# Kernel optimization log

Measured on AMD Instinct MI355X. Metric: run time of the kernel, lower is better.

The kernel has to match this reference:

```python
import jax, jax.numpy as jnp
import numpy as np
from jax import lax

B, C, H, W = 4, 256, 96, 96
DR, G, KS, RF = 4, 2, 3, 9.0
HID = C // DR          # 64
GC = HID // G          # 32 (group_channel)
SCALE = HID ** -0.5
MLP_H = C * 4          # 1024
EPS = 1e-5


def conv2d(x, w, b=None, groups=1):
    out = lax.conv_general_dilated(x, w, (1, 1), 'SAME',
                                   dimension_numbers=('NCHW', 'OIHW', 'NCHW'),
                                   feature_group_count=groups)
    return out if b is None else out + b[None, :, None, None]


def ln_chw(x, g, b):  # LayerNormProxy: layernorm over channel dim of NCHW
    m = x.mean(1, keepdims=True)
    v = ((x - m) ** 2).mean(1, keepdims=True)
    return (x - m) / jnp.sqrt(v + EPS) * g[None, :, None, None] + b[None, :, None, None]


def ln_last(x, g, b):
    m = x.mean(-1, keepdims=True)
    v = ((x - m) ** 2).mean(-1, keepdims=True)
    return (x - m) / jnp.sqrt(v + EPS) * g + b


def base_offset():
    pad = (KS - 1) // 2
    base = jnp.arange(-pad, pad + 1, dtype=jnp.float32)
    by = jnp.repeat(base, KS)
    bx = jnp.tile(base, KS)
    return jnp.stack([by, bx], 1).reshape(1, -1, 1, 1)  # [1, 2*KS*KS, 1, 1], (kh kw d) layout


def bilinear_zeros(img, ry, rx):
    # img [Cc,H,W]; ry,rx absolute pixel coords [Ho,Wo]; zero padding, align_corners=True
    Hh, Ww = img.shape[1], img.shape[2]
    y0 = jnp.floor(ry); x0 = jnp.floor(rx)
    wy = ry - y0; wx = rx - x0
    y0i = y0.astype(jnp.int32); x0i = x0.astype(jnp.int32)

    def corner(yi, xi, w):
        valid = (yi >= 0) & (yi < Hh) & (xi >= 0) & (xi < Ww)
        yc = jnp.clip(yi, 0, Hh - 1); xc = jnp.clip(xi, 0, Ww - 1)
        return img[:, yc, xc] * (w * valid)[None]

    return (corner(y0i, x0i, (1 - wy) * (1 - wx)) + corner(y0i, x0i + 1, (1 - wy) * wx)
            + corner(y0i + 1, x0i, wy * (1 - wx)) + corner(y0i + 1, x0i + 1, wy * wx))


def extract_feats(img, off):
    # img [(b g), Cc, H, W], off [(b g), 2*KS*KS, H, W] -> [(b g), KS*KS, Cc, H, W]
    Bg, Cc = img.shape[0], img.shape[1]
    off = off.reshape(Bg, KS, KS, 2, H, W).transpose(0, 1, 4, 2, 5, 3)  # b kh h kw w d
    iy, ix = jnp.meshgrid(jnp.arange(H, dtype=off.dtype), jnp.arange(W, dtype=off.dtype), indexing='ij')
    idx = jnp.stack([iy, ix], -1)  # [H, W, 2]
    coords = (off + idx[None, None, :, None]).reshape(Bg, KS * H, KS * W, 2)
    # torch normalizes to [-1,1] then grid_sample(align_corners=True) un-normalizes => absolute coords
    samp = jax.vmap(bilinear_zeros)(img, coords[..., 0], coords[..., 1])  # [Bg, Cc, KS*H, KS*W]
    return samp.reshape(Bg, Cc, KS, H, KS, W).transpose(0, 2, 4, 1, 3, 5).reshape(Bg, KS * KS, Cc, H, W)


def ldca_forward(x, y, g11, b11, g21, b21, g12, b12, w_qkv1, w_qkv2,
                 off1_dw_w, off1_ln_g, off1_ln_b, off1_w, off1_b,
                 off2_dw_w, off2_ln_g, off2_ln_b, off2_w, off2_b,
                 rpb, proj_w, proj_b, fc1_w, fc1_b, dw_w, dw_b, fc2_w, fc2_b):
    x_ = ln_chw(x, g11, b11)
    y_ = ln_chw(y, g21, b21)
    qkv1 = jnp.einsum('oc,bchw->bohw', w_qkv1, x_)   # [B, 3*HID, H, W]
    kv2c = jnp.einsum('oc,bchw->bohw', w_qkv2, y_)   # [B, 2*HID, H, W]
    q1 = qkv1[:, :HID].reshape(B * G, GC, H, W)

    def regroup(kv):  # b (d g c) h w -> (b g) (d c) h w
        return kv.reshape(B, 2, G, GC, H, W).transpose(0, 2, 1, 3, 4, 5).reshape(B * G, 2 * GC, H, W)

    kv1 = regroup(qkv1[:, HID:])
    kv2 = regroup(kv2c)

    bo = base_offset()

    def off_branch(dww, lng, lnb, w, b):
        t = conv2d(q1, dww, None, groups=GC)
        t = jax.nn.gelu(ln_chw(t, lng, lnb), approximate=False)
        return jnp.tanh(conv2d(t, w, b)) * RF + bo

    s1 = extract_feats(kv1, off_branch(off1_dw_w, off1_ln_g, off1_ln_b, off1_w, off1_b))
    s2 = extract_feats(kv2, off_branch(off2_dw_w, off2_ln_g, off2_ln_b, off2_w, off2_b))

    def to_kv(s):  # (b g) n (d c) h w -> d b (h w) n (g c)
        return s.reshape(B, G, KS * KS, 2, GC, H, W).transpose(3, 0, 5, 6, 2, 1, 4).reshape(2, B, H * W, KS * KS, G * GC)

    k1, v1 = to_kv(s1)
    k2, v2 = to_kv(s2)
    k = jnp.concatenate([k1 + rpb, k2 + rpb], 2)   # [B, HW, 2*KS*KS, HID]
    v = jnp.concatenate([v1, v2], 2)
    q = q1.reshape(B, G, GC, H, W).transpose(0, 3, 4, 1, 2).reshape(B, H * W, 1, G * GC) * SCALE
    attn = jax.nn.softmax(jnp.einsum('bnqd,bnkd->bnqk', q, k), axis=-1)
    o = jnp.einsum('bnqk,bnkd->bnqd', attn, v)[:, :, 0]  # [B, HW, HID]
    o = o @ proj_w.T + proj_b + x.transpose(0, 2, 3, 1).reshape(B, H * W, C)
    # MLP with depthwise-conv branch
    h = ln_last(o, g12, b12) @ fc1_w.T + fc1_b           # [B, HW, MLP_H]
    hd = conv2d(h.transpose(0, 2, 1).reshape(B, MLP_H, H, W), dw_w, dw_b, groups=MLP_H)
    hd = hd.reshape(B, MLP_H, H * W).transpose(0, 2, 1)
    h = jax.nn.gelu(h + hd, approximate=False)
    o = o + h @ fc2_w.T + fc2_b
    return o.reshape(B, H, W, C).transpose(0, 3, 1, 2)


def setup_inputs() -> dict:
    key = jax.random.key(0)
    keys = iter(jax.random.split(key, 40))

    def nrm(shape, s=0.02):
        return jax.random.normal(next(keys), shape, jnp.float32) * s

    inp = {
        'x': jax.random.normal(next(keys), (B, C, H, W), jnp.float32),
        'y': jax.random.normal(next(keys), (B, C, H, W), jnp.float32),
        'g11': jnp.ones((C,), jnp.float32), 'b11': jnp.zeros((C,), jnp.float32),
        'g21': jnp.ones((C,), jnp.float32), 'b21': jnp.zeros((C,), jnp.float32),
        'g12': jnp.ones((C,), jnp.float32), 'b12': jnp.zeros((C,), jnp.float32),
        'w_qkv1': nrm((3 * HID, C)), 'w_qkv2': nrm((2 * HID, C)),
        'off1_dw_w': nrm((GC, 1, 3, 3)),
        'off1_ln_g': jnp.ones((GC,), jnp.float32), 'off1_ln_b': jnp.zeros((GC,), jnp.float32),
        'off1_w': nrm((2 * KS * KS, GC, 3, 3)), 'off1_b': jnp.zeros((2 * KS * KS,), jnp.float32),
        'off2_dw_w': nrm((GC, 1, 3, 3)),
        'off2_ln_g': jnp.ones((GC,), jnp.float32), 'off2_ln_b': jnp.zeros((GC,), jnp.float32),
        'off2_w': nrm((2 * KS * KS, GC, 3, 3)), 'off2_b': jnp.zeros((2 * KS * KS,), jnp.float32),
        'rpb': nrm((1, 1, KS * KS, HID)),
        'proj_w': nrm((C, HID)), 'proj_b': jnp.zeros((C,), jnp.float32),
        'fc1_w': nrm((MLP_H, C)), 'fc1_b': jnp.zeros((MLP_H,), jnp.float32),
        'dw_w': nrm((MLP_H, 1, 3, 3)), 'dw_b': jnp.zeros((MLP_H,), jnp.float32),
        'fc2_w': nrm((C, MLP_H)), 'fc2_b': jnp.zeros((C,), jnp.float32),
    }
    return inp


def reference(x, y, g11, b11, g21, b21, g12, b12, w_qkv1, w_qkv2,
              off1_dw_w, off1_ln_g, off1_ln_b, off1_w, off1_b,
              off2_dw_w, off2_ln_g, off2_ln_b, off2_w, off2_b,
              rpb, proj_w, proj_b, fc1_w, fc1_b, dw_w, dw_b, fc2_w, fc2_b):
    return ldca_forward(x, y, g11, b11, g21, b21, g12, b12, w_qkv1, w_qkv2,
                        off1_dw_w, off1_ln_g, off1_ln_b, off1_w, off1_b,
                        off2_dw_w, off2_ln_g, off2_ln_b, off2_w, off2_b,
                        rpb, proj_w, proj_b, fc1_w, fc1_b, dw_w, dw_b, fc2_w, fc2_b)
```

## Files before the change

kernel.cpp:

```cpp
#include <hip/hip_runtime.h>
#include <math.h>


#define HH 96
#define WWD 96
#define HWP 9216
#define EPSV 1e-5f
#define RFV 9.0f

typedef unsigned short ushort;
typedef __attribute__((ext_vector_type(8))) short short8v;
typedef __attribute__((ext_vector_type(8))) ushort ushort8v;
typedef __attribute__((ext_vector_type(4))) float f32x4;

__device__ inline ushort f2bf(float f) {
  union { float f; unsigned u; } v; v.f = f;
  unsigned r = v.u + 0x7FFFu + ((v.u >> 16) & 1u);
  return (ushort)(r >> 16);
}
__device__ inline float bf2f(ushort h) {
  union { unsigned u; float f; } v; v.u = ((unsigned)h) << 16;
  return v.f;
}

__device__ inline void stf(float* p, float v) { *p = v; }
__device__ inline void stf(ushort* p, float v) { *p = f2bf(v); }

__device__ inline void stage16(const float* __restrict__ s, ushort* d) {
  const float4* s4 = (const float4*)s;
  float4 v0 = s4[0], v1 = s4[1], v2 = s4[2], v3 = s4[3];
  ushort8v r0, r1;
  r0[0] = f2bf(v0.x); r0[1] = f2bf(v0.y); r0[2] = f2bf(v0.z); r0[3] = f2bf(v0.w);
  r0[4] = f2bf(v1.x); r0[5] = f2bf(v1.y); r0[6] = f2bf(v1.z); r0[7] = f2bf(v1.w);
  r1[0] = f2bf(v2.x); r1[1] = f2bf(v2.y); r1[2] = f2bf(v2.z); r1[3] = f2bf(v2.w);
  r1[4] = f2bf(v3.x); r1[5] = f2bf(v3.y); r1[6] = f2bf(v3.z); r1[7] = f2bf(v3.w);
  ((ushort8v*)d)[0] = r0; ((ushort8v*)d)[1] = r1;
}
__device__ inline void stage16(const ushort* __restrict__ s, ushort* d) {
  ((ushort8v*)d)[0] = ((const ushort8v*)s)[0];
  ((ushort8v*)d)[1] = ((const ushort8v*)s)[1];
}

__global__ __launch_bounds__(256) void k_ln_stats(const float* __restrict__ in,
                                                  float* __restrict__ mout,
                                                  float* __restrict__ rout, int Cn) {
  int idx = blockIdx.x * 256 + threadIdx.x;
  int b = idx / HWP, p = idx % HWP;
  const float* base = in + (size_t)b * Cn * HWP + p;
  float s = 0.f, ss = 0.f;
  for (int c = 0; c < Cn; ++c) { float v = base[(size_t)c * HWP]; s += v; ss += v * v; }
  float m = s / (float)Cn;
  float var = ss / (float)Cn - m * m;
  mout[idx] = m;
  rout[idx] = rsqrtf(var + EPSV);
}

__global__ __launch_bounds__(256) void k_ln_stats_cc(const float* __restrict__ in,
                                                     float* __restrict__ mout,
                                                     float* __restrict__ rout) {
  int px = blockIdx.x * 4 + (threadIdx.x >> 6);
  int lane = threadIdx.x & 63;
  float4 v = *(const float4*)(in + (size_t)px * 256 + lane * 4);
  float s = v.x + v.y + v.z + v.w;
  float ss = v.x * v.x + v.y * v.y + v.z * v.z + v.w * v.w;
#pragma unroll
  for (int d = 1; d < 64; d <<= 1) { s += __shfl_xor(s, d); ss += __shfl_xor(ss, d); }
  if (lane == 0) {
    float m = s / 256.f;
    mout[px] = m;
    rout[px] = rsqrtf(ss / 256.f - m * m + EPSV);
  }
}

__global__ __launch_bounds__(256) void k_prepbf(const float* __restrict__ w,
                                                const float* __restrict__ g,
                                                const float* __restrict__ beta,
                                                ushort* __restrict__ wbf,
                                                float* __restrict__ sg, float* __restrict__ wb,
                                                int O, int K, int scaleRows) {
  int o = blockIdx.x * 4 + (threadIdx.x >> 6);
  int lane = threadIdx.x & 63;
  if (o >= O) return;
  float sc = (o < scaleRows) ? 0.125f : 1.f;
  float sgv = 0.f, wbv = 0.f;
  for (int c = lane; c < K; c += 64) {
    float wv = w[(size_t)o * K + c];
    float t = wv * (g ? g[c] : 1.f) * sc;
    ushort u = f2bf(t);
    wbf[(size_t)o * K + c] = u;
    sgv += bf2f(u);
    wbv += wv * (beta ? beta[c] : 0.f);
  }
#pragma unroll
  for (int d = 1; d < 64; d <<= 1) { sgv += __shfl_xor(sgv, d); wbv += __shfl_xor(wbv, d); }
  if (lane == 0) {
    if (sg) sg[o] = sgv;
    if (wb) wb[o] = wbv * sc;
  }
}

__global__ __launch_bounds__(256) void k_tocc(const float* __restrict__ src,
                                              ushort* __restrict__ dst) {
  __shared__ float tile[64][65];
  int tp = threadIdx.x & 63, tq = threadIdx.x >> 6;
  int p0 = blockIdx.x * 64, c0 = blockIdx.y * 64, b = blockIdx.z;
#pragma unroll 4
  for (int i = 0; i < 16; ++i) {
    int ch = tq * 16 + i;
    tile[ch][tp] = src[((size_t)b * 256 + c0 + ch) * HWP + p0 + tp];
  }
  __syncthreads();
#pragma unroll 4
  for (int i = 0; i < 16; ++i) {
    int pp = tq * 16 + i;
    dst[((size_t)b * HWP + p0 + pp) * 256 + c0 + tp] = f2bf(tile[tp][pp]);
  }
}

template <typename TI, typename TO, bool LNF, bool RES>
__global__ __launch_bounds__(256) void k_gemmB(const TI* __restrict__ act,
                                               const ushort* __restrict__ Wbf,
                                               const float* __restrict__ ms,
                                               const float* __restrict__ rs,
                                               const float* __restrict__ sg,
                                               const float* __restrict__ wb,
                                               const float* __restrict__ bias,
                                               const ushort* __restrict__ resid,
                                               TO* __restrict__ outp, int K, int O) {
  __shared__ ushort at[128][56];
  __shared__ ushort wt[64][56];
  int tid = threadIdx.x;
  int lane = tid & 63, wv = tid >> 6;
  int wr = wv >> 1, wc = wv & 1;
  int p0 = blockIdx.x * 128, o0 = blockIdx.y * 64, b = blockIdx.z;
  size_t pb = (size_t)b * HWP;
  int l15 = lane & 15, lk = (lane >> 4) * 8;
  f32x4 acc[4][2];
#pragma unroll
  for (int rt = 0; rt < 4; ++rt)
#pragma unroll
    for (int ct = 0; ct < 2; ++ct) { acc[rt][ct][0] = 0.f; acc[rt][ct][1] = 0.f; acc[rt][ct][2] = 0.f; acc[rt][ct][3] = 0.f; }

  for (int kb = 0; kb < K; kb += 32) {
    __syncthreads();
    {
      int p = tid >> 1, kh = (tid & 1) * 16;
      stage16(act + (pb + p0 + p) * (size_t)K + kb + kh, &at[p][kh]);
    }
    if (tid < 128) {
      int o = tid >> 1, kh = (tid & 1) * 16;
      stage16(Wbf + (size_t)(o0 + o) * K + kb + kh, &wt[o][kh]);
    }
    __syncthreads();
    short8v a[4], bb[2];
#pragma unroll
    for (int rt = 0; rt < 4; ++rt) a[rt] = *(const short8v*)&at[wr * 64 + rt * 16 + l15][lk];
#pragma unroll
    for (int ct = 0; ct < 2; ++ct) bb[ct] = *(const short8v*)&wt[wc * 32 + ct * 16 + l15][lk];
#pragma unroll
    for (int rt = 0; rt < 4; ++rt)
#pragma unroll
      for (int ct = 0; ct < 2; ++ct)
        acc[rt][ct] = __builtin_amdgcn_mfma_f32_16x16x32_bf16(a[rt], bb[ct], acc[rt][ct], 0, 0, 0);
  }
#pragma unroll
  for (int rt = 0; rt < 4; ++rt) {
    int pbase = p0 + wr * 64 + rt * 16 + (lane >> 4) * 4;
#pragma unroll
    for (int j = 0; j < 4; ++j) {
      int p = pbase + j;
      float rr = 0.f, mm = 0.f;
      if (LNF) { rr = rs[b * HWP + p]; mm = ms[b * HWP + p]; }
#pragma unroll
      for (int ct = 0; ct < 2; ++ct) {
        int o = o0 + wc * 32 + ct * 16 + l15;
        float v = acc[rt][ct][j];
        if (LNF) v = rr * v - rr * mm * sg[o];
        if (wb) v += wb[o];
        if (bias) v += bias[o];
        if (RES) v += bf2f(resid[(pb + p) * (size_t)O + o]);
        stf(&outp[(pb + p) * (size_t)O + o], v);
      }
    }
  }
}

__global__ __launch_bounds__(256) void k_q1p(const float* __restrict__ qkv1cc,
                                             float* __restrict__ q1p) {
  __shared__ float tile[64][65];
  int tp = threadIdx.x & 63, tq = threadIdx.x >> 6;
  int p0 = blockIdx.x * 64, b = blockIdx.y;
#pragma unroll 4
  for (int i = 0; i < 16; ++i) {
    int pp = tq * 16 + i;
    tile[tp][pp] = qkv1cc[((size_t)b * HWP + p0 + pp) * 192 + tp];
  }
  __syncthreads();
#pragma unroll 4
  for (int i = 0; i < 16; ++i) {
    int ch = tq * 16 + i;
    q1p[((size_t)b * 64 + ch) * HWP + p0 + tp] = tile[ch][tp] * 8.f;
  }
}

__global__ __launch_bounds__(256) void k_dw3x3(const float* __restrict__ q1p,
                                               const float* __restrict__ dww1,
                                               const float* __restrict__ dww2,
                                               float* __restrict__ t) {
  int p = blockIdx.x * 256 + threadIdx.x;
  int c = blockIdx.y, z = blockIdx.z;
  int bg = z & 7;
  int b = bg >> 1, g = bg & 1;
  const float* dww = (z >= 8) ? dww2 : dww1;
  int y = p / WWD, x = p % WWD;
  const float* src = q1p + ((size_t)b * 64 + g * 32 + c) * HWP;
  float acc = 0.f;
#pragma unroll
  for (int ky = 0; ky < 3; ++ky) {
    int yy = y + ky - 1;
    if (yy < 0 || yy >= HH) continue;
#pragma unroll
    for (int kx = 0; kx < 3; ++kx) {
      int xx = x + kx - 1;
      if (xx < 0 || xx >= WWD) continue;
      acc += src[yy * WWD + xx] * dww[c * 9 + ky * 3 + kx];
    }
  }
  t[(size_t)(z * 32 + c) * HWP + p] = acc;
}

__global__ __launch_bounds__(256) void k_ln_gelu32(float* __restrict__ t,
                                                   const float* __restrict__ g1,
                                                   const float* __restrict__ b1,
                                                   const float* __restrict__ g2,
                                                   const float* __restrict__ b2) {
  int idx = blockIdx.x * 256 + threadIdx.x;
  int z = idx / HWP, p = idx % HWP;
  const float* g = (z >= 8) ? g2 : g1;
  const float* bb = (z >= 8) ? b2 : b1;
  float* base = t + (size_t)z * 32 * HWP + p;
  float s = 0.f, ss = 0.f;
#pragma unroll
  for (int c = 0; c < 32; ++c) { float v = base[(size_t)c * HWP]; s += v; ss += v * v; }
  float m = s / 32.f;
  float var = ss / 32.f - m * m;
  float r = rsqrtf(var + EPSV);
#pragma unroll
  for (int c = 0; c < 32; ++c) {
    float v = base[(size_t)c * HWP];
    float xn = (v - m) * r * g[c] + bb[c];
    base[(size_t)c * HWP] = 0.5f * xn * (1.f + erff(xn * 0.70710678118654752f));
  }
}

__global__ __launch_bounds__(256) void k_conv18(const float* __restrict__ t,
                                                const float* __restrict__ w1,
                                                const float* __restrict__ b1,
                                                const float* __restrict__ w2,
                                                const float* __restrict__ b2,
                                                float* __restrict__ offo) {
  __shared__ float in_t[32 * 324];
  int tid = threadIdx.x;
  int tile = blockIdx.x, z = blockIdx.y;
  int ty0 = (tile / 6) * 16, tx0 = (tile % 6) * 16;
  const float* w = (z >= 8) ? w2 : w1;
  const float* bias = (z >= 8) ? b2 : b1;
  const float* tb = t + (size_t)z * 32 * HWP;
  for (int idx = tid; idx < 32 * 324; idx += 256) {
    int c = idx / 324, pp = idx % 324;
    int gy = ty0 - 1 + pp / 18, gx = tx0 - 1 + pp % 18;
    float v = 0.f;
    if (gy >= 0 && gy < HH && gx >= 0 && gx < WWD) v = tb[(size_t)c * HWP + gy * WWD + gx];
    in_t[idx] = v;
  }
  __syncthreads();
  int ly = tid >> 4, lx = tid & 15;
  float acc[18];
#pragma unroll
  for (int oc = 0; oc < 18; ++oc) acc[oc] = bias[oc];
  const float* basep = in_t + ly * 18 + lx;
  for (int c = 0; c < 32; ++c) {
#pragma unroll
    for (int dy = 0; dy < 3; ++dy)
#pragma unroll
      for (int dx = 0; dx < 3; ++dx) {
        float v = basep[c * 324 + dy * 18 + dx];
        int tap = c * 9 + dy * 3 + dx;
#pragma unroll
        for (int oc = 0; oc < 18; ++oc)
          acc[oc] = fmaf(v, w[oc * 288 + tap], acc[oc]);
      }
  }
  int p = (ty0 + ly) * WWD + tx0 + lx;
#pragma unroll
  for (int oc = 0; oc < 18; ++oc) {
    int n = oc >> 1, d = oc & 1;
    float basev = d ? (float)(n % 3 - 1) : (float)(n / 3 - 1);
    offo[((size_t)z * 18 + oc) * HWP + p] = tanhf(acc[oc]) * RFV + basev;
  }
}

__global__ __launch_bounds__(256) void k_attn(const float* __restrict__ qkv1cc,
                                              const float* __restrict__ kv2cc,
                                              const float* __restrict__ offo,
                                              const float* __restrict__ rpb,
                                              float* __restrict__ o_att) {
  __shared__ float rl[576];
  for (int i = threadIdx.x; i < 576; i += 256) rl[i] = rpb[i];
  __syncthreads();
  int pix = blockIdx.x * 4 + (threadIdx.x >> 6);
  int l = threadIdx.x & 63;
  int b = pix / HWP, p = pix % HWP;
  int y = p / WWD, x = p % WWD;
  int g = l >> 5;
  int bg = b * 2 + g;
  float qv = qkv1cc[((size_t)b * HWP + p) * 192 + l];
  float scores[18], vvv[18];
#pragma unroll
  for (int s = 0; s < 2; ++s) {
    const float* offp = offo + ((size_t)(s * 8 + bg) * 18) * HWP + p;
    const float* kvb = s ? (kv2cc + (size_t)b * HWP * 128) : (qkv1cc + (size_t)b * HWP * 192);
    int stride = s ? 128 : 192;
    int koff = s ? 0 : 64;
#pragma unroll
    for (int n = 0; n < 9; ++n) {
      float ry = (float)y + offp[(size_t)(2 * n) * HWP];
      float rx = (float)x + offp[(size_t)(2 * n + 1) * HWP];
      float y0f = floorf(ry), x0f = floorf(rx);
      float wy = ry - y0f, wx = rx - x0f;
      int y0 = (int)y0f, x0 = (int)x0f;
      float ka = 0.f, va = 0.f;
#pragma unroll
      for (int cy = 0; cy < 2; ++cy) {
        int yi = y0 + cy;
        if (yi < 0 || yi >= HH) continue;
        float wyc = cy ? wy : 1.f - wy;
#pragma unroll
        for (int cx = 0; cx < 2; ++cx) {
          int xi = x0 + cx;
          if (xi < 0 || xi >= WWD) continue;
          float wgt = wyc * (cx ? wx : 1.f - wx);
          const float* row = kvb + (size_t)(yi * WWD + xi) * stride + koff;
          ka += wgt * row[l];
          va += wgt * row[64 + l];
        }
      }
      float sp = qv * (ka + rl[n * 64 + l]);
      sp += __shfl_xor(sp, 1);
      sp += __shfl_xor(sp, 2);
      sp += __shfl_xor(sp, 4);
      sp += __shfl_xor(sp, 8);
      sp += __shfl_xor(sp, 16);
      sp += __shfl_xor(sp, 32);
      scores[s * 9 + n] = sp;
      vvv[s * 9 + n] = va;
    }
  }
  float mx = scores[0];
#pragma unroll
  for (int i = 1; i < 18; ++i) mx = fmaxf(mx, scores[i]);
  float sum = 0.f;
#pragma unroll
  for (int i = 0; i < 18; ++i) { scores[i] = expf(scores[i] - mx); sum += scores[i]; }
  float inv = 1.f / sum;
  float o = 0.f;
#pragma unroll
  for (int i = 0; i < 18; ++i) o += scores[i] * vvv[i];
  o_att[((size_t)b * HWP + p) * 64 + l] = o * inv;
}

__global__ __launch_bounds__(256) void k_dwgelu_cc(const ushort* __restrict__ h,
                                                   const float* __restrict__ w,
                                                   const float* __restrict__ bias,
                                                   ushort* __restrict__ h2) {
  __shared__ ushort tileh[324][48];
  __shared__ float wl[32][9];
  __shared__ float bl[32];
  int tid = threadIdx.x;
  int tile = blockIdx.x, chb = blockIdx.y, b = blockIdx.z;
  int ty0 = (tile / 6) * 16, tx0 = (tile % 6) * 16;
  size_t base = ((size_t)b * HWP) * 1024 + chb * 32;
  for (int i = tid; i < 288; i += 256) wl[i / 9][i % 9] = w[(chb * 32 + i / 9) * 9 + i % 9];
  if (tid < 32) bl[tid] = bias[chb * 32 + tid];
  for (int idx = tid; idx < 324; idx += 256) {
    int py = idx / 18, px = idx % 18;
    int gy = ty0 - 1 + py, gx = tx0 - 1 + px;
    ushort8v* d = (ushort8v*)&tileh[idx][0];
    if (gy >= 0 && gy < HH && gx >= 0 && gx < WWD) {
      const ushort8v* sv = (const ushort8v*)(h + base + (size_t)(gy * WWD + gx) * 1024);
      d[0] = sv[0]; d[1] = sv[1]; d[2] = sv[2]; d[3] = sv[3];
    } else {
      ushort8v z;
#pragma unroll
      for (int e = 0; e < 8; ++e) z[e] = 0;
      d[0] = z; d[1] = z; d[2] = z; d[3] = z;
    }
  }
  __syncthreads();
  int ly = tid >> 4, lx = tid & 15;
  float a[32];
#pragma unroll
  for (int c = 0; c < 32; ++c) a[c] = bl[c];
#pragma unroll
  for (int dy = 0; dy < 3; ++dy)
#pragma unroll
    for (int dx = 0; dx < 3; ++dx) {
      const ushort8v* t = (const ushort8v*)&tileh[(ly + dy) * 18 + lx + dx][0];
      int tap = dy * 3 + dx;
#pragma unroll
      for (int cq = 0; cq < 4; ++cq) {
        ushort8v vv = t[cq];
#pragma unroll
        for (int e = 0; e < 8; ++e) a[cq * 8 + e] += bf2f(vv[e]) * wl[cq * 8 + e][tap];
      }
    }
  const ushort8v* ctr = (const ushort8v*)&tileh[(ly + 1) * 18 + lx + 1][0];
  ushort8v* outv = (ushort8v*)(h2 + base + (size_t)((ty0 + ly) * WWD + tx0 + lx) * 1024);
#pragma unroll
  for (int cq = 0; cq < 4; ++cq) {
    ushort8v vv = ctr[cq];
    ushort8v rv;
#pragma unroll
    for (int e = 0; e < 8; ++e) {
      float v = bf2f(vv[e]) + a[cq * 8 + e];
      rv[e] = f2bf(0.5f * v * (1.f + erff(v * 0.70710678118654752f)));
    }
    outv[cq] = rv;
  }
}

__global__ __launch_bounds__(256) void k_fromcc(const float* __restrict__ fc2cc,
                                                const float* __restrict__ o1cc,
                                                float* __restrict__ outp) {
  __shared__ float tile[64][65];
  int tp = threadIdx.x & 63, tq = threadIdx.x >> 6;
  int p0 = blockIdx.x * 64, c0 = blockIdx.y * 64, b = blockIdx.z;
#pragma unroll 4
  for (int i = 0; i < 16; ++i) {
    int pp = tq * 16 + i;
    size_t idx = ((size_t)b * HWP + p0 + pp) * 256 + c0 + tp;
    tile[tp][pp] = fc2cc[idx] + o1cc[idx];
  }
  __syncthreads();
#pragma unroll 4
  for (int i = 0; i < 16; ++i) {
    int ch = tq * 16 + i;
    outp[((size_t)b * 256 + c0 + ch) * HWP + p0 + tp] = tile[ch][tp];
  }
}

extern "C" void kernel_launch(void* const* d_in, const int* in_sizes, int n_in,
                              void* d_out, int out_size, void* d_ws, size_t ws_size,
                              hipStream_t stream) {
  const float* x      = (const float*)d_in[0];
  const float* y      = (const float*)d_in[1];
  const float* g11    = (const float*)d_in[2];
  const float* b11    = (const float*)d_in[3];
  const float* g21    = (const float*)d_in[4];
  const float* b21    = (const float*)d_in[5];
  const float* g12    = (const float*)d_in[6];
  const float* b12    = (const float*)d_in[7];
  const float* w_qkv1 = (const float*)d_in[8];
  const float* w_qkv2 = (const float*)d_in[9];
  const float* o1dw   = (const float*)d_in[10];
  const float* o1lg   = (const float*)d_in[11];
  const float* o1lb   = (const float*)d_in[12];
  const float* o1w    = (const float*)d_in[13];
  const float* o1bi   = (const float*)d_in[14];
  const float* o2dw   = (const float*)d_in[15];
  const float* o2lg   = (const float*)d_in[16];
  const float* o2lb   = (const float*)d_in[17];
  const float* o2w    = (const float*)d_in[18];
  const float* o2bi   = (const float*)d_in[19];
  const float* rpb    = (const float*)d_in[20];
  const float* proj_w = (const float*)d_in[21];
  const float* proj_b = (const float*)d_in[22];
  const float* fc1_w  = (const float*)d_in[23];
  const float* fc1_b  = (const float*)d_in[24];
  const float* dw_w   = (const float*)d_in[25];
  const float* dw_b   = (const float*)d_in[26];
  const float* fc2_w  = (const float*)d_in[27];
  const float* fc2_b  = (const float*)d_in[28];
  float* out = (float*)d_out;

  float* ws = (float*)d_ws;
  ushort* xcc   = (ushort*)(ws + 0);
  ushort* ycc   = (ushort*)(ws + 4718592);
  float*  q1p   = ws + 4718592;
  float*  qkv1cc= ws + 9437184;
  float*  kv2cc = ws + 16515072;
  float*  offb  = ws + 21233664;
  float*  o_att = ws + 23887872;
  float*  tbuf12= ws + 26247168;
  ushort* hcc   = (ushort*)(ws + 0);
  ushort* h2cc  = (ushort*)(ws + 18874368);
  float*  o1cc  = ws + 37748736;
  float*  fc2cc = ws + 0;
  const size_t SW = 47185920;
  float* m_x = ws + SW, *r_x = m_x + 36864, *m_y = r_x + 36864, *r_y = m_y + 36864;
  float* m_o = r_y + 36864, *r_o = m_o + 36864;
  ushort* Wg1bf = (ushort*)(ws + SW + 221184);
  float* sg1 = ws + SW + 245760, *wb1 = sg1 + 192;
  ushort* Wg2bf = (ushort*)(ws + SW + 246144);
  float* sg2 = ws + SW + 262528, *wb2 = sg2 + 128;
  ushort* Wgfbf = (ushort*)(ws + SW + 262784);
  float* sgf = ws + SW + 393856, *wbf = sgf + 1024;
  ushort* projbf = (ushort*)(ws + SW + 395904);
  ushort* fc2bf  = (ushort*)(ws + SW + 404096);

  k_prepbf<<<48, 256, 0, stream>>>(w_qkv1, g11, b11, Wg1bf, sg1, wb1, 192, 256, 64);
  k_prepbf<<<32, 256, 0, stream>>>(w_qkv2, g21, b21, Wg2bf, sg2, wb2, 128, 256, 0);
  k_prepbf<<<256, 256, 0, stream>>>(fc1_w, g12, b12, Wgfbf, sgf, wbf, 1024, 256, 0);
  k_prepbf<<<64, 256, 0, stream>>>(proj_w, nullptr, nullptr, projbf, nullptr, nullptr, 256, 64, 0);
  k_prepbf<<<64, 256, 0, stream>>>(fc2_w, nullptr, nullptr, fc2bf, nullptr, nullptr, 256, 1024, 0);

  k_ln_stats<<<144, 256, 0, stream>>>(x, m_x, r_x, 256);
  k_ln_stats<<<144, 256, 0, stream>>>(y, m_y, r_y, 256);
  k_tocc<<<dim3(144, 4, 4), 256, 0, stream>>>(x, xcc);
  k_tocc<<<dim3(144, 4, 4), 256, 0, stream>>>(y, ycc);

  k_gemmB<ushort, float, true, false><<<dim3(72, 3, 4), 256, 0, stream>>>(
      xcc, Wg1bf, m_x, r_x, sg1, wb1, nullptr, nullptr, qkv1cc, 256, 192);
  k_gemmB<ushort, float, true, false><<<dim3(72, 2, 4), 256, 0, stream>>>(
      ycc, Wg2bf, m_y, r_y, sg2, wb2, nullptr, nullptr, kv2cc, 256, 128);

  k_q1p<<<dim3(144, 4), 256, 0, stream>>>(qkv1cc, q1p);
  k_dw3x3<<<dim3(36, 32, 16), 256, 0, stream>>>(q1p, o1dw, o2dw, tbuf12);
  k_ln_gelu32<<<576, 256, 0, stream>>>(tbuf12, o1lg, o1lb, o2lg, o2lb);
  k_conv18<<<dim3(36, 16), 256, 0, stream>>>(tbuf12, o1w, o1bi, o2w, o2bi, offb);

  k_attn<<<9216, 256, 0, stream>>>(qkv1cc, kv2cc, offb, rpb, o_att);

  k_gemmB<float, float, false, true><<<dim3(72, 4, 4), 256, 0, stream>>>(
      o_att, projbf, nullptr, nullptr, nullptr, nullptr, proj_b, xcc, o1cc, 64, 256);

  k_ln_stats_cc<<<9216, 256, 0, stream>>>(o1cc, m_o, r_o);
  k_gemmB<float, ushort, true, false><<<dim3(72, 16, 4), 256, 0, stream>>>(
      o1cc, Wgfbf, m_o, r_o, sgf, wbf, fc1_b, nullptr, hcc, 256, 1024);
  k_dwgelu_cc<<<dim3(36, 32, 4), 256, 0, stream>>>(hcc, dw_w, dw_b, h2cc);
  k_gemmB<ushort, float, false, false><<<dim3(72, 4, 4), 256, 0, stream>>>(
      h2cc, fc2bf, nullptr, nullptr, nullptr, nullptr, fc2_b, nullptr, fc2cc, 1024, 256);

  k_fromcc<<<dim3(144, 4, 4), 256, 0, stream>>>(fc2cc, o1cc, out);
}
```

Baseline: 1.074 ms.

## Pack K/V as bf16 pairs for attention gather and widen GEMM output tiles

Adds a packing kernel that converts the K and V channels of both streams into interleaved bf16 pairs, so each bilinear corner fetch in the attention kernel is one 32-bit load instead of two strided fp32 loads. The attention output is stored as bf16, which halves its write and the proj GEMM's read. The GEMM gains a CT template parameter that lets most launches use 128-wide output tiles, reusing each activation tile across twice as many outputs and halving the grid along O. This costs an extra pass to pack K/V, adds bf16 rounding error to K/V and the attention output, and raises accumulator register use in the wider GEMMs.

After: 1.117 ms. +4.0%, slower.

```diff
diff --git a/kernel.cpp b/kernel.cpp
--- a/kernel.cpp
+++ b/kernel.cpp
@@ -9,6 +9,7 @@
 #define RFV 9.0f
 
 typedef unsigned short ushort;
+typedef unsigned int uint;
 typedef __attribute__((ext_vector_type(8))) short short8v;
 typedef __attribute__((ext_vector_type(8))) ushort ushort8v;
 typedef __attribute__((ext_vector_type(4))) float f32x4;
@@ -117,7 +118,7 @@
   }
 }
 
-template <typename TI, typename TO, bool LNF, bool RES>
+template <typename TI, typename TO, bool LNF, bool RES, int CT>
 __global__ __launch_bounds__(256) void k_gemmB(const TI* __restrict__ act,
                                                const ushort* __restrict__ Wbf,
                                                const float* __restrict__ ms,
@@ -128,18 +129,18 @@
                                                const ushort* __restrict__ resid,
                                                TO* __restrict__ outp, int K, int O) {
   __shared__ ushort at[128][56];
-  __shared__ ushort wt[64][56];
+  __shared__ ushort wt[32 * CT][56];
   int tid = threadIdx.x;
   int lane = tid & 63, wv = tid >> 6;
   int wr = wv >> 1, wc = wv & 1;
-  int p0 = blockIdx.x * 128, o0 = blockIdx.y * 64, b = blockIdx.z;
+  int p0 = blockIdx.x * 128, o0 = blockIdx.y * (32 * CT), b = blockIdx.z;
   size_t pb = (size_t)b * HWP;
   int l15 = lane & 15, lk = (lane >> 4) * 8;
-  f32x4 acc[4][2];
+  f32x4 acc[4][CT];
 #pragma unroll
   for (int rt = 0; rt < 4; ++rt)
 #pragma unroll
-    for (int ct = 0; ct < 2; ++ct) { acc[rt][ct][0] = 0.f; acc[rt][ct][1] = 0.f; acc[rt][ct][2] = 0.f; acc[rt][ct][3] = 0.f; }
+    for (int ct = 0; ct < CT; ++ct) { acc[rt][ct][0] = 0.f; acc[rt][ct][1] = 0.f; acc[rt][ct][2] = 0.f; acc[rt][ct][3] = 0.f; }
 
   for (int kb = 0; kb < K; kb += 32) {
     __syncthreads();
@@ -147,20 +148,23 @@
       int p = tid >> 1, kh = (tid & 1) * 16;
       stage16(act + (pb + p0 + p) * (size_t)K + kb + kh, &at[p][kh]);
     }
-    if (tid < 128) {
+    if (CT == 4) {
       int o = tid >> 1, kh = (tid & 1) * 16;
       stage16(Wbf + (size_t)(o0 + o) * K + kb + kh, &wt[o][kh]);
+    } else if (tid < 128) {
+      int o = tid >> 1, kh = (tid & 1) * 16;
+      stage16(Wbf + (size_t)(o0 + o) * K + kb + kh, &wt[o][kh]);
     }
     __syncthreads();
-    short8v a[4], bb[2];
+    short8v a[4], bb[CT];
 #pragma unroll
     for (int rt = 0; rt < 4; ++rt) a[rt] = *(const short8v*)&at[wr * 64 + rt * 16 + l15][lk];
 #pragma unroll
-    for (int ct = 0; ct < 2; ++ct) bb[ct] = *(const short8v*)&wt[wc * 32 + ct * 16 + l15][lk];
+    for (int ct = 0; ct < CT; ++ct) bb[ct] = *(const short8v*)&wt[wc * (16 * CT) + ct * 16 + l15][lk];
 #pragma unroll
     for (int rt = 0; rt < 4; ++rt)
 #pragma unroll
-      for (int ct = 0; ct < 2; ++ct)
+      for (int ct = 0; ct < CT; ++ct)
         acc[rt][ct] = __builtin_amdgcn_mfma_f32_16x16x32_bf16(a[rt], bb[ct], acc[rt][ct], 0, 0, 0);
   }
 #pragma unroll
@@ -172,8 +176,8 @@
       float rr = 0.f, mm = 0.f;
       if (LNF) { rr = rs[b * HWP + p]; mm = ms[b * HWP + p]; }
 #pragma unroll
-      for (int ct = 0; ct < 2; ++ct) {
-        int o = o0 + wc * 32 + ct * 16 + l15;
+      for (int ct = 0; ct < CT; ++ct) {
+        int o = o0 + wc * (16 * CT) + ct * 16 + l15;
         float v = acc[rt][ct][j];
         if (LNF) v = rr * v - rr * mm * sg[o];
         if (wb) v += wb[o];
@@ -201,6 +205,19 @@
     int ch = tq * 16 + i;
     q1p[((size_t)b * 64 + ch) * HWP + p0 + tp] = tile[ch][tp] * 8.f;
   }
+}
+
+__global__ __launch_bounds__(256) void k_packkv(const float* __restrict__ qkv1cc,
+                                                const float* __restrict__ kv2cc,
+                                                uint* __restrict__ kvpack) {
+  int pix = blockIdx.x * 4 + (threadIdx.x >> 6);
+  int l = threadIdx.x & 63;
+  const float* r1 = qkv1cc + (size_t)pix * 192;
+  kvpack[(size_t)pix * 64 + l] =
+      (uint)f2bf(r1[64 + l]) | ((uint)f2bf(r1[128 + l]) << 16);
+  const float* r2 = kv2cc + (size_t)pix * 128;
+  kvpack[((size_t)4 * HWP + pix) * 64 + l] =
+      (uint)f2bf(r2[l]) | ((uint)f2bf(r2[64 + l]) << 16);
 }
 
 __global__ __launch_bounds__(256) void k_dw3x3(const float* __restrict__ q1p,
@@ -301,10 +318,10 @@
 }
 
 __global__ __launch_bounds__(256) void k_attn(const float* __restrict__ qkv1cc,
-                                              const float* __restrict__ kv2cc,
+                                              const uint* __restrict__ kvpack,
                                               const float* __restrict__ offo,
                                               const float* __restrict__ rpb,
-                                              float* __restrict__ o_att) {
+                                              ushort* __restrict__ o_att) {
   __shared__ float rl[576];
   for (int i = threadIdx.x; i < 576; i += 256) rl[i] = rpb[i];
   __syncthreads();
@@ -319,9 +336,7 @@
 #pragma unroll
   for (int s = 0; s < 2; ++s) {
     const float* offp = offo + ((size_t)(s * 8 + bg) * 18) * HWP + p;
-    const float* kvb = s ? (kv2cc + (size_t)b * HWP * 128) : (qkv1cc + (size_t)b * HWP * 192);
-    int stride = s ? 128 : 192;
-    int koff = s ? 0 : 64;
+    const uint* kvb = kvpack + ((size_t)(s * 4 + b) * HWP) * 64;
 #pragma unroll
     for (int n = 0; n < 9; ++n) {
       float ry = (float)y + offp[(size_t)(2 * n) * HWP];
@@ -340,9 +355,9 @@
           int xi = x0 + cx;
           if (xi < 0 || xi >= WWD) continue;
           float wgt = wyc * (cx ? wx : 1.f - wx);
-          const float* row = kvb + (size_t)(yi * WWD + xi) * stride + koff;
-          ka += wgt * row[l];
-          va += wgt * row[64 + l];
+          uint kv = kvb[(size_t)(yi * WWD + xi) * 64 + l];
+          ka += wgt * bf2f((ushort)(kv & 0xFFFFu));
+          va += wgt * bf2f((ushort)(kv >> 16));
         }
       }
       float sp = qv * (ka + rl[n * 64 + l]);
@@ -366,7 +381,7 @@
   float o = 0.f;
 #pragma unroll
   for (int i = 0; i < 18; ++i) o += scores[i] * vvv[i];
-  o_att[((size_t)b * HWP + p) * 64 + l] = o * inv;
+  o_att[((size_t)b * HWP + p) * 64 + l] = f2bf(o * inv);
 }
 
 __global__ __launch_bounds__(256) void k_dwgelu_cc(const ushort* __restrict__ h,
@@ -490,8 +505,9 @@
   float*  qkv1cc= ws + 9437184;
   float*  kv2cc = ws + 16515072;
   float*  offb  = ws + 21233664;
-  float*  o_att = ws + 23887872;
+  ushort* o_att = (ushort*)(ws + 23887872);
   float*  tbuf12= ws + 26247168;
+  uint*   kvpack= (uint*)(ws + 30965760);
   ushort* hcc   = (ushort*)(ws + 0);
   ushort* h2cc  = (ushort*)(ws + 18874368);
   float*  o1cc  = ws + 37748736;
@@ -519,26 +535,27 @@
   k_tocc<<<dim3(144, 4, 4), 256, 0, stream>>>(x, xcc);
   k_tocc<<<dim3(144, 4, 4), 256, 0, stream>>>(y, ycc);
 
-  k_gemmB<ushort, float, true, false><<<dim3(72, 3, 4), 256, 0, stream>>>(
+  k_gemmB<ushort, float, true, false, 2><<<dim3(72, 3, 4), 256, 0, stream>>>(
       xcc, Wg1bf, m_x, r_x, sg1, wb1, nullptr, nullptr, qkv1cc, 256, 192);
-  k_gemmB<ushort, float, true, false><<<dim3(72, 2, 4), 256, 0, stream>>>(
+  k_gemmB<ushort, float, true, false, 4><<<dim3(72, 1, 4), 256, 0, stream>>>(
       ycc, Wg2bf, m_y, r_y, sg2, wb2, nullptr, nullptr, kv2cc, 256, 128);
 
   k_q1p<<<dim3(144, 4), 256, 0, stream>>>(qkv1cc, q1p);
+  k_packkv<<<9216, 256, 0, stream>>>(qkv1cc, kv2cc, kvpack);
   k_dw3x3<<<dim3(36, 32, 16), 256, 0, stream>>>(q1p, o1dw, o2dw, tbuf12);
   k_ln_gelu32<<<576, 256, 0, stream>>>(tbuf12, o1lg, o1lb, o2lg, o2lb);
   k_conv18<<<dim3(36, 16), 256, 0, stream>>>(tbuf12, o1w, o1bi, o2w, o2bi, offb);
 
-  k_attn<<<9216, 256, 0, stream>>>(qkv1cc, kv2cc, offb, rpb, o_att);
-
-  k_gemmB<float, float, false, true><<<dim3(72, 4, 4), 256, 0, stream>>>(
+  k_attn<<<9216, 256, 0, stream>>>(qkv1cc, kvpack, offb, rpb, o_att);
+
+  k_gemmB<ushort, float, false, true, 4><<<dim3(72, 2, 4), 256, 0, stream>>>(
       o_att, projbf, nullptr, nullptr, nullptr, nullptr, proj_b, xcc, o1cc, 64, 256);
 
   k_ln_stats_cc<<<9216, 256, 0, stream>>>(o1cc, m_o, r_o);
-  k_gemmB<float, ushort, true, false><<<dim3(72, 16, 4), 256, 0, stream>>>(
+  k_gemmB<float, ushort, true, false, 4><<<dim3(72, 8, 4), 256, 0, stream>>>(
       o1cc, Wgfbf, m_o, r_o, sgf, wbf, fc1_b, nullptr, hcc, 256, 1024);
   k_dwgelu_cc<<<dim3(36, 32, 4), 256, 0, stream>>>(hcc, dw_w, dw_b, h2cc);
-  k_gemmB<ushort, float, false, false><<<dim3(72, 4, 4), 256, 0, stream>>>(
+  k_gemmB<ushort, float, false, false, 4><<<dim3(72, 2, 4), 256, 0, stream>>>(
       h2cc, fc2bf, nullptr, nullptr, nullptr, nullptr, fc2_b, nullptr, fc2cc, 1024, 256);
 
   k_fromcc<<<dim3(144, 4, 4), 256, 0, stream>>>(fc2cc, o1cc, out);
```
